# Performance work log

Hardware: AMD Instinct MI355X
Metric: run time of the kernel (lower is better)

## Reference

```python
import jax, jax.numpy as jnp
import numpy as np
from jax.scipy.linalg import expm

S = 64          # alphabet size (codons)
M = 8           # number of models, prod(model_shape)
N_LEAVES = 32   # leaves of the balanced binary tree
N_EDGES = 62    # nodes 0..62, every non-root node has one parent edge (edge id == child node id)
B = 1024        # batch (alignment columns)
# per-level ranges of child-node ids; node 32+j has children (2j, 2j+1), etc.
LEVELS = [(0, 32), (32, 48), (48, 56), (56, 60), (60, 62)]


def inv_stereographic_projection(p):
    # maps R^{s-1} -> unit sphere S^{s-1}
    n2 = jnp.sum(p * p, axis=-1, keepdims=True)
    return jnp.concatenate([2.0 * p / (n2 + 1.0), (n2 - 1.0) / (n2 + 1.0)], axis=-1)


def generator(R, pi):
    # R: (M, s(s-1)/2) exchangeabilities, pi: (M, s) stationary distribution
    iu, ju = np.triu_indices(S, 1)
    A = jnp.zeros((M, S, S), R.dtype).at[:, iu, ju].set(R).at[:, ju, iu].set(R)
    Q = A * pi[:, None, :]                       # Q_ij = A_ij * pi_j (off-diagonal)
    row = jnp.sum(Q, axis=-1)                    # (M, S)
    return Q - jnp.eye(S, dtype=Q.dtype) * row[:, :, None]


def felsenstein(leave_configuration, R_inv, pi_inv, lengths):
    pi = inv_stereographic_projection(pi_inv) ** 2           # (M, S), rows sum to 1
    R = jnp.exp(R_inv)                                       # positive rates
    Q = generator(R, pi)                                     # (M, S, S)
    tQ = lengths[:, None, None, None] * Q[None]              # (E, M, S, S)
    P = jax.vmap(expm)(tQ.reshape(-1, S, S)).reshape(N_EDGES, M, S, S)
    # leaf alphas: tile leaf observations over the M models -> (n_leaves, B, M, S)
    prev = jnp.broadcast_to(
        leave_configuration.transpose(1, 0, 2)[:, :, None, :],
        (N_LEAVES, leave_configuration.shape[0], M, S))
    # level-synchronous pruning: messages up each parent edge, then product of the two children
    for a, b in LEVELS:
        msg = jnp.einsum('emcd,ebmd->ebmc', P[a:b], prev)    # per-edge transition
        prev = msg[0::2] * msg[1::2]                         # combine sibling pairs
    root = prev[0]                                           # (B, M, S)
    out = jnp.einsum('bms,ms->bm', root, pi)                 # P(data | model m)
    return out.reshape(out.shape[0], M)                      # (B, *model_shape)


def setup_inputs() -> dict:
    key = jax.random.key(0)
    k1, k2, k3, k4 = jax.random.split(key, 4)
    leave_configuration = jax.random.uniform(k1, (B, N_LEAVES, S), dtype=jnp.float32)
    tree_indices = jnp.zeros((B,), dtype=jnp.int32)          # single tree (F=1)
    R_inv = jax.random.uniform(k2, (M, S * (S - 1) // 2), dtype=jnp.float32,
                               minval=-1.0, maxval=1.0)
    pi_inv = jnp.full((M, S - 1), 1.0 / (np.sqrt(S) - 1.0), dtype=jnp.float32) \
        + 0.01 * jax.random.normal(k3, (M, S - 1), dtype=jnp.float32)
    lengths = jax.random.uniform(k4, (N_EDGES,), dtype=jnp.float32,
                                 minval=0.05, maxval=0.5)
    return {'leave_configuration': leave_configuration, 'R_inv': R_inv,
            'pi_inv': pi_inv, 'lengths': lengths, 'tree_indices': tree_indices}


def reference(leave_configuration, R_inv, pi_inv, lengths, tree_indices):
    # F=1: tf.dynamic_partition/gather_nd batch slicing is the identity, so
    # tree_indices is closed over / unused.
    return felsenstein(leave_configuration, R_inv, pi_inv, lengths)
```

## Files before the change

kernel.cpp:

```cpp
#include <hip/hip_runtime.h>

typedef unsigned short u16;
typedef unsigned int u32;
typedef __attribute__((ext_vector_type(8))) __bf16 bf16x8;
typedef __attribute__((ext_vector_type(4))) float f32x4;

constexpr size_t OFF_PI  = 0;
constexpr size_t OFF_PBH = 512;
constexpr size_t OFF_PBL = OFF_PBH + 1015808;

union FR { uint4 u; bf16x8 v; };

__device__ __forceinline__ void split_bf16(float x, u16& h, u16& l) {
  u32 b = __float_as_uint(x);
  u32 hb = (b + 0x7fffu + ((b >> 16) & 1u)) & 0xffff0000u;
  h = (u16)(hb >> 16);
  float r = x - __uint_as_float(hb);
  l = (u16)(__float_as_uint(r) >> 16);
}

__device__ __forceinline__ void split8(const f32x4 a, const f32x4 b,
                                       uint4& hi, uint4& lo) {
  u16 h[8], l[8];
  split_bf16(a.x, h[0], l[0]); split_bf16(a.y, h[1], l[1]);
  split_bf16(a.z, h[2], l[2]); split_bf16(a.w, h[3], l[3]);
  split_bf16(b.x, h[4], l[4]); split_bf16(b.y, h[5], l[5]);
  split_bf16(b.z, h[6], l[6]); split_bf16(b.w, h[7], l[7]);
  hi.x = h[0] | ((u32)h[1] << 16); hi.y = h[2] | ((u32)h[3] << 16);
  hi.z = h[4] | ((u32)h[5] << 16); hi.w = h[6] | ((u32)h[7] << 16);
  lo.x = l[0] | ((u32)l[1] << 16); lo.y = l[2] | ((u32)l[3] << 16);
  lo.z = l[4] | ((u32)l[5] << 16); lo.w = l[6] | ((u32)l[7] << 16);
}

__device__ __forceinline__ void mfma3(f32x4& a, const uint4 ah, const uint4 al,
                                      const uint4 bh, const uint4 bl) {
  FR Ah, Al, Bh, Bl;
  Ah.u = ah; Al.u = al; Bh.u = bh; Bl.u = bl;
  a = __builtin_amdgcn_mfma_f32_16x16x32_bf16(Ah.v, Bh.v, a, 0, 0, 0);
  a = __builtin_amdgcn_mfma_f32_16x16x32_bf16(Ah.v, Bl.v, a, 0, 0, 0);
  a = __builtin_amdgcn_mfma_f32_16x16x32_bf16(Al.v, Bh.v, a, 0, 0, 0);
}

__device__ __forceinline__ void xt_read2(const u32* b, int row, int chunk,
                                         uint4& hi, uint4& lo) {
  const int dw = (row << 5) + (((chunk + row) & 7) << 2);
  hi = *(const uint4*)&b[dw];
  lo = *(const uint4*)&b[2048 + dw];
}
__device__ __forceinline__ void xt_write4(u32* b, int row, int cp, int half,
                                          const f32x4 v) {
  u16 h[4], l[4];
  split_bf16(v.x, h[0], l[0]); split_bf16(v.y, h[1], l[1]);
  split_bf16(v.z, h[2], l[2]); split_bf16(v.w, h[3], l[3]);
  const int dw = (row << 5) + (((cp + row) & 7) << 2) + half * 2;
  uint2 hh, ll;
  hh.x = h[0] | ((u32)h[1] << 16); hh.y = h[2] | ((u32)h[3] << 16);
  ll.x = l[0] | ((u32)l[1] << 16); ll.y = l[2] | ((u32)l[3] << 16);
  *(uint2*)&b[dw] = hh;
  *(uint2*)&b[2048 + dw] = ll;
}

__global__ __launch_bounds__(1024) void k_pcomb(
    const float* __restrict__ R_inv, const float* __restrict__ pi_inv,
    const float* __restrict__ lengths, float* __restrict__ ws,
    u16* __restrict__ PBH, u16* __restrict__ PBL) {
  const int m = blockIdx.x & 7, prt = blockIdx.x >> 3;
  const int tid = threadIdx.x, lane = tid & 63, w = tid >> 6;
  const int ln = lane & 15, kq = lane >> 4;
  __shared__ float pis[64];
  __shared__ float n2s;
  __shared__ __align__(16) float Qs[64 * 68];
  __shared__ __align__(16) u32 PB[8][4096];

  if (tid < 64) {
    float p = (tid < 63) ? pi_inv[m * 63 + tid] : 0.f;
    float v = p * p;
    #pragma unroll
    for (int off = 32; off; off >>= 1) v += __shfl_down(v, off, 64);
    if (tid == 0) n2s = v;
  }
  __syncthreads();
  if (tid < 64) {
    const float den = n2s + 1.f;
    const float x = (tid < 63) ? 2.f * pi_inv[m * 63 + tid] / den
                               : (n2s - 1.f) / den;
    const float pv = x * x;
    pis[tid] = pv;
    if (prt == 0) ws[OFF_PI + (size_t)m * 64 + tid] = pv;
  }
  __syncthreads();
  for (int idx = tid; idx < 4096; idx += 1024) {
    const int i = idx >> 6, j = idx & 63;
    float q = 0.f;
    if (i != j) {
      const int a = min(i, j), b = max(i, j);
      const int kk = a * (127 - a) / 2 + (b - a - 1);
      q = expf(R_inv[m * 2016 + kk]) * pis[j];
    }
    Qs[i * 68 + j] = q;
  }
  __syncthreads();
  if (tid < 64) {
    float s = 0.f;
    #pragma unroll 4
    for (int j4 = 0; j4 < 64; j4 += 4) {
      const f32x4 q = *(const f32x4*)&Qs[tid * 68 + j4];
      s += q.x + q.y + q.z + q.w;
    }
    Qs[tid * 68 + tid] = -s;
  }
  __syncthreads();
  float q[12][4];
  const int ci0 = tid >> 4, cj0 = (tid & 15) * 4;
  #pragma unroll
  for (int r = 0; r < 4; ++r) q[0][r] = Qs[ci0 * 68 + cj0 + r];
  if (tid < 512) {
    const int i = tid >> 3, c = tid & 7;
    const f32x4 a = *(const f32x4*)&Qs[i * 68 + c * 8];
    const f32x4 b = *(const f32x4*)&Qs[i * 68 + c * 8 + 4];
    uint4 h, l;
    split8(a, b, h, l);
    const int dw = (i << 5) + (((c + i) & 7) << 2);
    *(uint4*)&PB[0][dw] = h;
    *(uint4*)&PB[0][2048 + dw] = l;
  } else {
    const int t2 = tid - 512, j = t2 >> 3, c = t2 & 7;
    f32x4 a, b;
    a.x = Qs[(c * 8 + 0) * 68 + j]; a.y = Qs[(c * 8 + 1) * 68 + j];
    a.z = Qs[(c * 8 + 2) * 68 + j]; a.w = Qs[(c * 8 + 3) * 68 + j];
    b.x = Qs[(c * 8 + 4) * 68 + j]; b.y = Qs[(c * 8 + 5) * 68 + j];
    b.z = Qs[(c * 8 + 6) * 68 + j]; b.w = Qs[(c * 8 + 7) * 68 + j];
    uint4 h, l;
    split8(a, b, h, l);
    const int dw = (j << 5) + (((c + j) & 7) << 2);
    *(uint4*)&PB[4][dw] = h;
    *(uint4*)&PB[4][2048 + dw] = l;
  }
  __syncthreads();

  const f32x4 z = {0.f, 0.f, 0.f, 0.f};
  const int ct = w >> 2, bt = w & 3;
  auto mm = [&](const u32* RX, const u32* CY, u32* dstC, u32* dstR) {
    uint4 ah[2], al[2], bh[2], bl[2];
    #pragma unroll
    for (int kh = 0; kh < 2; ++kh) {
      xt_read2(RX, ct * 16 + ln, kh * 4 + kq, ah[kh], al[kh]);
      xt_read2(CY, bt * 16 + ln, kh * 4 + kq, bh[kh], bl[kh]);
    }
    f32x4 a = z;
    #pragma unroll
    for (int kh = 0; kh < 2; ++kh) mfma3(a, ah[kh], al[kh], bh[kh], bl[kh]);
    #pragma unroll
    for (int r = 0; r < 4; ++r)
      Qs[(ct * 16 + kq * 4 + r) * 64 + bt * 16 + ln] = a[r];
    if (dstC) xt_write4(dstC, bt * 16 + ln, 2 * ct + (kq >> 1), kq & 1, a);
    if (dstR) {
      #pragma unroll
      for (int kh = 0; kh < 2; ++kh) {
        xt_read2(CY, ct * 16 + ln, kh * 4 + kq, ah[kh], al[kh]);
        xt_read2(RX, bt * 16 + ln, kh * 4 + kq, bh[kh], bl[kh]);
      }
      f32x4 a2 = z;
      #pragma unroll
      for (int kh = 0; kh < 2; ++kh) mfma3(a2, ah[kh], al[kh], bh[kh], bl[kh]);
      xt_write4(dstR, bt * 16 + ln, 2 * ct + (kq >> 1), kq & 1, a2);
    }
  };
  auto step = [&](const u32* RX, const u32* CY, int k, u32* dstC, u32* dstR) {
    mm(RX, CY, dstC, dstR);
    __syncthreads();
    #pragma unroll
    for (int r = 0; r < 4; ++r) q[k - 1][r] = Qs[tid * 4 + r];
    __syncthreads();
  };
  step(PB[0], PB[4], 2, PB[5], PB[1]);
  step(PB[1], PB[4], 3, PB[6], nullptr);
  step(PB[1], PB[5], 4, PB[7], PB[2]);
  step(PB[2], PB[4], 5, nullptr, nullptr);
  step(PB[2], PB[5], 6, nullptr, nullptr);
  step(PB[2], PB[6], 7, nullptr, nullptr);
  step(PB[2], PB[7], 8, nullptr, PB[3]);
  step(PB[3], PB[4], 9, nullptr, nullptr);
  step(PB[3], PB[5], 10, nullptr, nullptr);
  step(PB[3], PB[6], 11, nullptr, nullptr);
  step(PB[3], PB[7], 12, nullptr, nullptr);

  #pragma unroll
  for (int ei = 0; ei < 4; ++ei) {
    const int e = prt * 4 + ei;
    if (e >= 62) break;
    const float t = lengths[e];
    float av[4] = {0.f, 0.f, 0.f, 0.f};
    const int dr = ci0 - cj0;
    if (dr >= 0 && dr < 4) av[dr] = 1.f;
    float cf = 1.f;
    #pragma unroll
    for (int k = 1; k <= 12; ++k) {
      cf *= t / (float)k;
      #pragma unroll
      for (int r = 0; r < 4; ++r) av[r] = fmaf(cf, q[k - 1][r], av[r]);
    }
    u16 h[4], l[4];
    split_bf16(av[0], h[0], l[0]); split_bf16(av[1], h[1], l[1]);
    split_bf16(av[2], h[2], l[2]); split_bf16(av[3], h[3], l[3]);
    const size_t base = (((size_t)e * 8 + m) << 12) + tid * 4;
    ushort4 h4, l4;
    h4.x = h[0]; h4.y = h[1]; h4.z = h[2]; h4.w = h[3];
    l4.x = l[0]; l4.y = l[1]; l4.z = l[2]; l4.w = l[3];
    *(ushort4*)(PBH + base) = h4;
    *(ushort4*)(PBL + base) = l4;
  }
}

__global__ __launch_bounds__(512, 2) void k_tree(
    const float* __restrict__ leaves, const u16* __restrict__ Phi,
    const u16* __restrict__ Plo, const float* __restrict__ ws,
    float* __restrict__ out) {
  const int m = blockIdx.x & 7, btile = blockIdx.x >> 3;
  const int tid = threadIdx.x, lane = tid & 63, w = tid >> 6;
  const int ln = lane & 15, kq = lane >> 4;
  __shared__ __align__(16) u32 slots[16 * 2048];
  __shared__ float psum[2][4][16];
  const f32x4 z = {0.f, 0.f, 0.f, 0.f};

  auto node_read = [&](int slot, int row, int kh, uint4& bh, uint4& bl) {
    const int jc = kh * 8 + kq * 2;
    const u32* b = &slots[slot * 2048 + row * 64];
    const uint4 A = *(const uint4*)&b[((jc + row) & 15) << 2];
    const uint4 B = *(const uint4*)&b[((jc + 1 + row) & 15) << 2];
    bh.x = A.x; bh.y = A.y; bh.z = B.x; bh.w = B.y;
    bl.x = A.z; bl.y = A.w; bl.z = B.z; bl.w = B.w;
  };
  auto node_write = [&](int slot, int row, int jc, const f32x4 v) {
    u16 h[4], l[4];
    split_bf16(v.x, h[0], l[0]); split_bf16(v.y, h[1], l[1]);
    split_bf16(v.z, h[2], l[2]); split_bf16(v.w, h[3], l[3]);
    uint4 pk;
    pk.x = h[0] | ((u32)h[1] << 16); pk.y = h[2] | ((u32)h[3] << 16);
    pk.z = l[0] | ((u32)l[1] << 16); pk.w = l[2] | ((u32)l[3] << 16);
    *(uint4*)&slots[slot * 2048 + row * 64 + (((jc + row) & 15) << 2)] = pk;
  };

  auto do_pair = [&](int eb, int p, int s0, int s1, int outSlot, int bt0,
                     int nbt, int ct0, int nct, bool leaf, f32x4* rootout) {
    uint4 bfh[2][2][2], bfl[2][2][2];
    #pragma unroll
    for (int s = 0; s < 2; ++s)
      #pragma unroll
      for (int bi = 0; bi < 2; ++bi) {
        if (bi >= nbt) continue;
        const int row = (bt0 + bi) * 16 + ln;
        #pragma unroll
        for (int kh = 0; kh < 2; ++kh) {
          if (leaf) {
            const float* g = leaves + (size_t)(btile * 32 + row) * 2048 +
                             (size_t)(eb + 2 * p + s) * 64 + kh * 32 + kq * 8;
            const f32x4 xa = *(const f32x4*)g;
            const f32x4 xb = *(const f32x4*)(g + 4);
            split8(xa, xb, bfh[s][bi][kh], bfl[s][bi][kh]);
          } else {
            node_read(s ? s1 : s0, row, kh, bfh[s][bi][kh], bfl[s][bi][kh]);
          }
        }
      }
    uint4 ph[2][4][2], pl[2][4][2];
    #pragma unroll
    for (int s = 0; s < 2; ++s) {
      const size_t pb = ((size_t)(eb + 2 * p + s) * 8 + m) << 12;
      #pragma unroll
      for (int ci = 0; ci < 4; ++ci) {
        if (ci >= nct) continue;
        #pragma unroll
        for (int kh = 0; kh < 2; ++kh) {
          const size_t off =
              pb + (size_t)((ct0 + ci) * 16 + ln) * 64 + kh * 32 + kq * 8;
          ph[s][ci][kh] = *(const uint4*)(Phi + off);
          pl[s][ci][kh] = *(const uint4*)(Plo + off);
        }
      }
    }
    f32x4 a0[4][2];
    #pragma unroll
    for (int ci = 0; ci < 4; ++ci) {
      if (ci >= nct) continue;
      #pragma unroll
      for (int bi = 0; bi < 2; ++bi) {
        if (bi >= nbt) continue;
        f32x4 a = z;
        #pragma unroll
        for (int kh = 0; kh < 2; ++kh)
          mfma3(a, ph[0][ci][kh], pl[0][ci][kh], bfh[0][bi][kh], bfl[0][bi][kh]);
        a0[ci][bi] = a;
      }
    }
    #pragma unroll
    for (int ci = 0; ci < 4; ++ci) {
      if (ci >= nct) continue;
      #pragma unroll
      for (int bi = 0; bi < 2; ++bi) {
        if (bi >= nbt) continue;
        f32x4 a = z;
        #pragma unroll
        for (int kh = 0; kh < 2; ++kh)
          mfma3(a, ph[1][ci][kh], pl[1][ci][kh], bfh[1][bi][kh], bfl[1][bi][kh]);
        const f32x4 pr = a0[ci][bi] * a;
        if (rootout)
          *rootout = pr;
        else
          node_write(outSlot, (bt0 + bi) * 16 + ln, (ct0 + ci) * 4 + kq, pr);
      }
    }
  };

  do_pair(0, w, -1, -1, w, 0, 2, 0, 4, true, nullptr);
  do_pair(0, w + 8, -1, -1, w + 8, 0, 2, 0, 4, true, nullptr);
  __syncthreads();
  do_pair(32, w, 2 * w, 2 * w + 1, 2 * w, 0, 2, 0, 4, false, nullptr);
  __syncthreads();
  {
    const int j = w >> 1, bi = w & 1;
    do_pair(48, j, 4 * j, 4 * j + 2, 4 * j, bi, 1, 0, 4, false, nullptr);
  }
  __syncthreads();
  {
    const int j = w >> 2, bi = w & 1, ch = (w >> 1) & 1;
    do_pair(56, j, 8 * j, 8 * j + 4, 8 * j + 1, bi, 1, ch * 2, 2, false,
            nullptr);
  }
  __syncthreads();
  {
    f32x4 pr = z;
    do_pair(60, 0, 1, 9, -1, w & 1, 1, w >> 1, 1, false, &pr);
    const f32x4 piv =
        *(const f32x4*)&ws[OFF_PI + (size_t)m * 64 + (w >> 1) * 16 + kq * 4];
    float v = pr.x * piv.x + pr.y * piv.y + pr.z * piv.z + pr.w * piv.w;
    v += __shfl_xor(v, 16, 64);
    v += __shfl_xor(v, 32, 64);
    if (lane < 16) psum[w & 1][w >> 1][lane] = v;
  }
  __syncthreads();
  if (tid < 32) {
    const int bi = tid >> 4, bb = tid & 15;
    out[(size_t)(btile * 32 + tid) * 8 + m] =
        psum[bi][0][bb] + psum[bi][1][bb] + psum[bi][2][bb] + psum[bi][3][bb];
  }
}

extern "C" void kernel_launch(void* const* d_in, const int* in_sizes, int n_in,
                              void* d_out, int out_size, void* d_ws, size_t ws_size,
                              hipStream_t stream) {
  const float* leaves  = (const float*)d_in[0];
  const float* R_inv   = (const float*)d_in[1];
  const float* pi_inv  = (const float*)d_in[2];
  const float* lengths = (const float*)d_in[3];
  float* out = (float*)d_out;
  float* ws  = (float*)d_ws;

  u16* PBH = (u16*)(ws + OFF_PBH);
  u16* PBL = (u16*)(ws + OFF_PBL);

  hipLaunchKernelGGL(k_pcomb, dim3(128), dim3(1024), 0, stream, R_inv, pi_inv,
                     lengths, ws, PBH, PBL);
  hipLaunchKernelGGL(k_tree, dim3(256), dim3(512), 0, stream, leaves, PBH, PBL,
                     ws, out);
}
```

Baseline: 123.9 us.

## Halve batch tile per block to double grid and raise occupancy

The tree kernel now handles 16 batch columns per block instead of 32, so the grid doubles to 512 blocks. Shared memory slots are halved and launch bounds ask for 4 blocks per CU. The upper tree levels are re-split across warps by output column quarter instead of batch half. More parallelism and occupancy should hide latency better, but each block reloads the P matrices for half as many columns, doubling P global/L2 traffic.

```diff
diff --git a/kernel.cpp b/kernel.cpp
--- a/kernel.cpp
+++ b/kernel.cpp
@@ -212,20 +212,20 @@
   }
 }
 
-__global__ __launch_bounds__(512, 2) void k_tree(
+__global__ __launch_bounds__(512, 4) void k_tree(
     const float* __restrict__ leaves, const u16* __restrict__ Phi,
     const u16* __restrict__ Plo, const float* __restrict__ ws,
     float* __restrict__ out) {
   const int m = blockIdx.x & 7, btile = blockIdx.x >> 3;
   const int tid = threadIdx.x, lane = tid & 63, w = tid >> 6;
   const int ln = lane & 15, kq = lane >> 4;
-  __shared__ __align__(16) u32 slots[16 * 2048];
-  __shared__ float psum[2][4][16];
+  __shared__ __align__(16) u32 slots[16 * 1024];
+  __shared__ float psum[4][16];
   const f32x4 z = {0.f, 0.f, 0.f, 0.f};
 
   auto node_read = [&](int slot, int row, int kh, uint4& bh, uint4& bl) {
     const int jc = kh * 8 + kq * 2;
-    const u32* b = &slots[slot * 2048 + row * 64];
+    const u32* b = &slots[slot * 1024 + row * 64];
     const uint4 A = *(const uint4*)&b[((jc + row) & 15) << 2];
     const uint4 B = *(const uint4*)&b[((jc + 1 + row) & 15) << 2];
     bh.x = A.x; bh.y = A.y; bh.z = B.x; bh.w = B.y;
@@ -238,29 +238,24 @@
     uint4 pk;
     pk.x = h[0] | ((u32)h[1] << 16); pk.y = h[2] | ((u32)h[3] << 16);
     pk.z = l[0] | ((u32)l[1] << 16); pk.w = l[2] | ((u32)l[3] << 16);
-    *(uint4*)&slots[slot * 2048 + row * 64 + (((jc + row) & 15) << 2)] = pk;
-  };
-
-  auto do_pair = [&](int eb, int p, int s0, int s1, int outSlot, int bt0,
-                     int nbt, int ct0, int nct, bool leaf, f32x4* rootout) {
-    uint4 bfh[2][2][2], bfl[2][2][2];
+    *(uint4*)&slots[slot * 1024 + row * 64 + (((jc + row) & 15) << 2)] = pk;
+  };
+
+  auto do_pair = [&](int eb, int p, int s0, int s1, int outSlot, int ct0,
+                     int nct, bool leaf, f32x4* rootout) {
+    uint4 bfh[2][2], bfl[2][2];
     #pragma unroll
     for (int s = 0; s < 2; ++s)
       #pragma unroll
-      for (int bi = 0; bi < 2; ++bi) {
-        if (bi >= nbt) continue;
-        const int row = (bt0 + bi) * 16 + ln;
-        #pragma unroll
-        for (int kh = 0; kh < 2; ++kh) {
-          if (leaf) {
-            const float* g = leaves + (size_t)(btile * 32 + row) * 2048 +
-                             (size_t)(eb + 2 * p + s) * 64 + kh * 32 + kq * 8;
-            const f32x4 xa = *(const f32x4*)g;
-            const f32x4 xb = *(const f32x4*)(g + 4);
-            split8(xa, xb, bfh[s][bi][kh], bfl[s][bi][kh]);
-          } else {
-            node_read(s ? s1 : s0, row, kh, bfh[s][bi][kh], bfl[s][bi][kh]);
-          }
+      for (int kh = 0; kh < 2; ++kh) {
+        if (leaf) {
+          const float* g = leaves + (size_t)(btile * 16 + ln) * 2048 +
+                           (size_t)(eb + 2 * p + s) * 64 + kh * 32 + kq * 8;
+          const f32x4 xa = *(const f32x4*)g;
+          const f32x4 xb = *(const f32x4*)(g + 4);
+          split8(xa, xb, bfh[s][kh], bfl[s][kh]);
+        } else {
+          node_read(s ? s1 : s0, ln, kh, bfh[s][kh], bfl[s][kh]);
         }
       }
     uint4 ph[2][4][2], pl[2][4][2];
@@ -279,70 +274,60 @@
         }
       }
     }
-    f32x4 a0[4][2];
+    f32x4 a0[4];
     #pragma unroll
     for (int ci = 0; ci < 4; ++ci) {
       if (ci >= nct) continue;
-      #pragma unroll
-      for (int bi = 0; bi < 2; ++bi) {
-        if (bi >= nbt) continue;
-        f32x4 a = z;
-        #pragma unroll
-        for (int kh = 0; kh < 2; ++kh)
-          mfma3(a, ph[0][ci][kh], pl[0][ci][kh], bfh[0][bi][kh], bfl[0][bi][kh]);
-        a0[ci][bi] = a;
-      }
+      f32x4 a = z;
+      #pragma unroll
+      for (int kh = 0; kh < 2; ++kh)
+        mfma3(a, ph[0][ci][kh], pl[0][ci][kh], bfh[0][kh], bfl[0][kh]);
+      a0[ci] = a;
     }
     #pragma unroll
     for (int ci = 0; ci < 4; ++ci) {
       if (ci >= nct) continue;
-      #pragma unroll
-      for (int bi = 0; bi < 2; ++bi) {
-        if (bi >= nbt) continue;
-        f32x4 a = z;
-        #pragma unroll
-        for (int kh = 0; kh < 2; ++kh)
-          mfma3(a, ph[1][ci][kh], pl[1][ci][kh], bfh[1][bi][kh], bfl[1][bi][kh]);
-        const f32x4 pr = a0[ci][bi] * a;
-        if (rootout)
-          *rootout = pr;
-        else
-          node_write(outSlot, (bt0 + bi) * 16 + ln, (ct0 + ci) * 4 + kq, pr);
-      }
-    }
-  };
-
-  do_pair(0, w, -1, -1, w, 0, 2, 0, 4, true, nullptr);
-  do_pair(0, w + 8, -1, -1, w + 8, 0, 2, 0, 4, true, nullptr);
-  __syncthreads();
-  do_pair(32, w, 2 * w, 2 * w + 1, 2 * w, 0, 2, 0, 4, false, nullptr);
+      f32x4 a = z;
+      #pragma unroll
+      for (int kh = 0; kh < 2; ++kh)
+        mfma3(a, ph[1][ci][kh], pl[1][ci][kh], bfh[1][kh], bfl[1][kh]);
+      const f32x4 pr = a0[ci] * a;
+      if (rootout)
+        *rootout = pr;
+      else
+        node_write(outSlot, ln, (ct0 + ci) * 4 + kq, pr);
+    }
+  };
+
+  do_pair(0, w, -1, -1, w, 0, 4, true, nullptr);
+  do_pair(0, w + 8, -1, -1, w + 8, 0, 4, true, nullptr);
+  __syncthreads();
+  do_pair(32, w, 2 * w, 2 * w + 1, 2 * w, 0, 4, false, nullptr);
   __syncthreads();
   {
-    const int j = w >> 1, bi = w & 1;
-    do_pair(48, j, 4 * j, 4 * j + 2, 4 * j, bi, 1, 0, 4, false, nullptr);
+    const int j = w >> 1, ch = w & 1;
+    do_pair(48, j, 4 * j, 4 * j + 2, 4 * j + 1, ch * 2, 2, false, nullptr);
   }
   __syncthreads();
   {
-    const int j = w >> 2, bi = w & 1, ch = (w >> 1) & 1;
-    do_pair(56, j, 8 * j, 8 * j + 4, 8 * j + 1, bi, 1, ch * 2, 2, false,
-            nullptr);
-  }
-  __syncthreads();
-  {
+    const int j = w >> 2, cq = w & 3;
+    do_pair(56, j, 8 * j + 1, 8 * j + 5, 8 * j + 3, cq, 1, false, nullptr);
+  }
+  __syncthreads();
+  if (w < 4) {
     f32x4 pr = z;
-    do_pair(60, 0, 1, 9, -1, w & 1, 1, w >> 1, 1, false, &pr);
+    do_pair(60, 0, 3, 11, -1, w, 1, false, &pr);
     const f32x4 piv =
-        *(const f32x4*)&ws[OFF_PI + (size_t)m * 64 + (w >> 1) * 16 + kq * 4];
+        *(const f32x4*)&ws[OFF_PI + (size_t)m * 64 + w * 16 + kq * 4];
     float v = pr.x * piv.x + pr.y * piv.y + pr.z * piv.z + pr.w * piv.w;
     v += __shfl_xor(v, 16, 64);
     v += __shfl_xor(v, 32, 64);
-    if (lane < 16) psum[w & 1][w >> 1][lane] = v;
-  }
-  __syncthreads();
-  if (tid < 32) {
-    const int bi = tid >> 4, bb = tid & 15;
-    out[(size_t)(btile * 32 + tid) * 8 + m] =
-        psum[bi][0][bb] + psum[bi][1][bb] + psum[bi][2][bb] + psum[bi][3][bb];
+    if (lane < 16) psum[w][lane] = v;
+  }
+  __syncthreads();
+  if (tid < 16) {
+    out[(size_t)(btile * 16 + tid) * 8 + m] =
+        psum[0][tid] + psum[1][tid] + psum[2][tid] + psum[3][tid];
   }
 }
 
@@ -361,6 +346,6 @@
 
   hipLaunchKernelGGL(k_pcomb, dim3(128), dim3(1024), 0, stream, R_inv, pi_inv,
                      lengths, ws, PBH, PBL);
-  hipLaunchKernelGGL(k_tree, dim3(256), dim3(512), 0, stream, leaves, PBH, PBL,
+  hipLaunchKernelGGL(k_tree, dim3(512), dim3(512), 0, stream, leaves, PBH, PBL,
                      ws, out);
 }
```

After: 147.0 us. 18.6% more time.

## Halve k_pcomb block size and double grid to spread edges across more blocks

Applied to the files above, without the earlier changes.

Changes k_pcomb from 128 blocks of 1024 threads to 256 blocks of 512 threads. Each thread now handles two of the former thread tiles in the power-series matrix multiplies and Taylor accumulation. Each block evaluates 2 edges instead of 4. This spreads the per-edge work over more CUs, but every block still recomputes Q and its 12 powers, so the redundant prologue work doubles. Register use also grows because q is now 12x8.

```diff
diff --git a/kernel.cpp b/kernel.cpp
--- a/kernel.cpp
+++ b/kernel.cpp
@@ -60,7 +60,7 @@
   *(uint2*)&b[2048 + dw] = ll;
 }
 
-__global__ __launch_bounds__(1024) void k_pcomb(
+__global__ __launch_bounds__(512, 2) void k_pcomb(
     const float* __restrict__ R_inv, const float* __restrict__ pi_inv,
     const float* __restrict__ lengths, float* __restrict__ ws,
     u16* __restrict__ PBH, u16* __restrict__ PBL) {
@@ -89,7 +89,7 @@
     if (prt == 0) ws[OFF_PI + (size_t)m * 64 + tid] = pv;
   }
   __syncthreads();
-  for (int idx = tid; idx < 4096; idx += 1024) {
+  for (int idx = tid; idx < 4096; idx += 512) {
     const int i = idx >> 6, j = idx & 63;
     float q = 0.f;
     if (i != j) {
@@ -110,11 +110,15 @@
     Qs[tid * 68 + tid] = -s;
   }
   __syncthreads();
-  float q[12][4];
-  const int ci0 = tid >> 4, cj0 = (tid & 15) * 4;
+  float q[12][8];
   #pragma unroll
-  for (int r = 0; r < 4; ++r) q[0][r] = Qs[ci0 * 68 + cj0 + r];
-  if (tid < 512) {
+  for (int g = 0; g < 2; ++g) {
+    const int vt = tid + 512 * g;
+    const int ci0 = vt >> 4, cj0 = (vt & 15) * 4;
+    #pragma unroll
+    for (int r = 0; r < 4; ++r) q[0][g * 4 + r] = Qs[ci0 * 68 + cj0 + r];
+  }
+  {
     const int i = tid >> 3, c = tid & 7;
     const f32x4 a = *(const f32x4*)&Qs[i * 68 + c * 8];
     const f32x4 b = *(const f32x4*)&Qs[i * 68 + c * 8 + 4];
@@ -123,54 +127,60 @@
     const int dw = (i << 5) + (((c + i) & 7) << 2);
     *(uint4*)&PB[0][dw] = h;
     *(uint4*)&PB[0][2048 + dw] = l;
-  } else {
-    const int t2 = tid - 512, j = t2 >> 3, c = t2 & 7;
-    f32x4 a, b;
-    a.x = Qs[(c * 8 + 0) * 68 + j]; a.y = Qs[(c * 8 + 1) * 68 + j];
-    a.z = Qs[(c * 8 + 2) * 68 + j]; a.w = Qs[(c * 8 + 3) * 68 + j];
-    b.x = Qs[(c * 8 + 4) * 68 + j]; b.y = Qs[(c * 8 + 5) * 68 + j];
-    b.z = Qs[(c * 8 + 6) * 68 + j]; b.w = Qs[(c * 8 + 7) * 68 + j];
-    uint4 h, l;
-    split8(a, b, h, l);
-    const int dw = (j << 5) + (((c + j) & 7) << 2);
+    const int j = i;
+    f32x4 ca, cb;
+    ca.x = Qs[(c * 8 + 0) * 68 + j]; ca.y = Qs[(c * 8 + 1) * 68 + j];
+    ca.z = Qs[(c * 8 + 2) * 68 + j]; ca.w = Qs[(c * 8 + 3) * 68 + j];
+    cb.x = Qs[(c * 8 + 4) * 68 + j]; cb.y = Qs[(c * 8 + 5) * 68 + j];
+    cb.z = Qs[(c * 8 + 6) * 68 + j]; cb.w = Qs[(c * 8 + 7) * 68 + j];
+    split8(ca, cb, h, l);
     *(uint4*)&PB[4][dw] = h;
     *(uint4*)&PB[4][2048 + dw] = l;
   }
   __syncthreads();
 
   const f32x4 z = {0.f, 0.f, 0.f, 0.f};
-  const int ct = w >> 2, bt = w & 3;
   auto mm = [&](const u32* RX, const u32* CY, u32* dstC, u32* dstR) {
-    uint4 ah[2], al[2], bh[2], bl[2];
-    #pragma unroll
-    for (int kh = 0; kh < 2; ++kh) {
-      xt_read2(RX, ct * 16 + ln, kh * 4 + kq, ah[kh], al[kh]);
-      xt_read2(CY, bt * 16 + ln, kh * 4 + kq, bh[kh], bl[kh]);
-    }
-    f32x4 a = z;
-    #pragma unroll
-    for (int kh = 0; kh < 2; ++kh) mfma3(a, ah[kh], al[kh], bh[kh], bl[kh]);
-    #pragma unroll
-    for (int r = 0; r < 4; ++r)
-      Qs[(ct * 16 + kq * 4 + r) * 64 + bt * 16 + ln] = a[r];
-    if (dstC) xt_write4(dstC, bt * 16 + ln, 2 * ct + (kq >> 1), kq & 1, a);
-    if (dstR) {
+    #pragma unroll
+    for (int tt = 0; tt < 2; ++tt) {
+      const int T = w + tt * 8;
+      const int ct = T >> 2, bt = T & 3;
+      uint4 ah[2], al[2], bh[2], bl[2];
       #pragma unroll
       for (int kh = 0; kh < 2; ++kh) {
-        xt_read2(CY, ct * 16 + ln, kh * 4 + kq, ah[kh], al[kh]);
-        xt_read2(RX, bt * 16 + ln, kh * 4 + kq, bh[kh], bl[kh]);
-      }
-      f32x4 a2 = z;
-      #pragma unroll
-      for (int kh = 0; kh < 2; ++kh) mfma3(a2, ah[kh], al[kh], bh[kh], bl[kh]);
-      xt_write4(dstR, bt * 16 + ln, 2 * ct + (kq >> 1), kq & 1, a2);
+        xt_read2(RX, ct * 16 + ln, kh * 4 + kq, ah[kh], al[kh]);
+        xt_read2(CY, bt * 16 + ln, kh * 4 + kq, bh[kh], bl[kh]);
+      }
+      f32x4 a = z;
+      #pragma unroll
+      for (int kh = 0; kh < 2; ++kh) mfma3(a, ah[kh], al[kh], bh[kh], bl[kh]);
+      #pragma unroll
+      for (int r = 0; r < 4; ++r)
+        Qs[(ct * 16 + kq * 4 + r) * 64 + bt * 16 + ln] = a[r];
+      if (dstC) xt_write4(dstC, bt * 16 + ln, 2 * ct + (kq >> 1), kq & 1, a);
+      if (dstR) {
+        uint4 ch[2], cl[2], dh[2], dl[2];
+        #pragma unroll
+        for (int kh = 0; kh < 2; ++kh) {
+          xt_read2(CY, ct * 16 + ln, kh * 4 + kq, ch[kh], cl[kh]);
+          xt_read2(RX, bt * 16 + ln, kh * 4 + kq, dh[kh], dl[kh]);
+        }
+        f32x4 a2 = z;
+        #pragma unroll
+        for (int kh = 0; kh < 2; ++kh) mfma3(a2, ch[kh], cl[kh], dh[kh], dl[kh]);
+        xt_write4(dstR, bt * 16 + ln, 2 * ct + (kq >> 1), kq & 1, a2);
+      }
     }
   };
   auto step = [&](const u32* RX, const u32* CY, int k, u32* dstC, u32* dstR) {
     mm(RX, CY, dstC, dstR);
     __syncthreads();
     #pragma unroll
-    for (int r = 0; r < 4; ++r) q[k - 1][r] = Qs[tid * 4 + r];
+    for (int g = 0; g < 2; ++g) {
+      const int vt = tid + 512 * g;
+      #pragma unroll
+      for (int r = 0; r < 4; ++r) q[k - 1][g * 4 + r] = Qs[vt * 4 + r];
+    }
     __syncthreads();
   };
   step(PB[0], PB[4], 2, PB[5], PB[1]);
@@ -186,29 +196,39 @@
   step(PB[3], PB[7], 12, nullptr, nullptr);
 
   #pragma unroll
-  for (int ei = 0; ei < 4; ++ei) {
-    const int e = prt * 4 + ei;
+  for (int ei = 0; ei < 2; ++ei) {
+    const int e = prt * 2 + ei;
     if (e >= 62) break;
     const float t = lengths[e];
-    float av[4] = {0.f, 0.f, 0.f, 0.f};
-    const int dr = ci0 - cj0;
-    if (dr >= 0 && dr < 4) av[dr] = 1.f;
+    float av[8] = {0.f, 0.f, 0.f, 0.f, 0.f, 0.f, 0.f, 0.f};
+    #pragma unroll
+    for (int g = 0; g < 2; ++g) {
+      const int vt = tid + 512 * g;
+      const int dr = (vt >> 4) - ((vt & 15) * 4);
+      if (dr >= 0 && dr < 4) av[g * 4 + dr] = 1.f;
+    }
     float cf = 1.f;
     #pragma unroll
     for (int k = 1; k <= 12; ++k) {
       cf *= t / (float)k;
       #pragma unroll
-      for (int r = 0; r < 4; ++r) av[r] = fmaf(cf, q[k - 1][r], av[r]);
-    }
-    u16 h[4], l[4];
-    split_bf16(av[0], h[0], l[0]); split_bf16(av[1], h[1], l[1]);
-    split_bf16(av[2], h[2], l[2]); split_bf16(av[3], h[3], l[3]);
-    const size_t base = (((size_t)e * 8 + m) << 12) + tid * 4;
-    ushort4 h4, l4;
-    h4.x = h[0]; h4.y = h[1]; h4.z = h[2]; h4.w = h[3];
-    l4.x = l[0]; l4.y = l[1]; l4.z = l[2]; l4.w = l[3];
-    *(ushort4*)(PBH + base) = h4;
-    *(ushort4*)(PBL + base) = l4;
+      for (int r = 0; r < 8; ++r) av[r] = fmaf(cf, q[k - 1][r], av[r]);
+    }
+    #pragma unroll
+    for (int g = 0; g < 2; ++g) {
+      const int vt = tid + 512 * g;
+      u16 h[4], l[4];
+      split_bf16(av[g * 4 + 0], h[0], l[0]);
+      split_bf16(av[g * 4 + 1], h[1], l[1]);
+      split_bf16(av[g * 4 + 2], h[2], l[2]);
+      split_bf16(av[g * 4 + 3], h[3], l[3]);
+      const size_t base = (((size_t)e * 8 + m) << 12) + (size_t)vt * 4;
+      ushort4 h4, l4;
+      h4.x = h[0]; h4.y = h[1]; h4.z = h[2]; h4.w = h[3];
+      l4.x = l[0]; l4.y = l[1]; l4.z = l[2]; l4.w = l[3];
+      *(ushort4*)(PBH + base) = h4;
+      *(ushort4*)(PBL + base) = l4;
+    }
   }
 }
 
@@ -359,7 +379,7 @@
   u16* PBH = (u16*)(ws + OFF_PBH);
   u16* PBL = (u16*)(ws + OFF_PBL);
 
-  hipLaunchKernelGGL(k_pcomb, dim3(128), dim3(1024), 0, stream, R_inv, pi_inv,
+  hipLaunchKernelGGL(k_pcomb, dim3(256), dim3(512), 0, stream, R_inv, pi_inv,
                      lengths, ws, PBH, PBL);
   hipLaunchKernelGGL(k_tree, dim3(256), dim3(512), 0, stream, leaves, PBH, PBL,
                      ws, out);
```

Result: no change. 122.5 us (-1.2%).
